# Optimization experiments

Hardware: AMD Instinct MI355X
Metric: run time of the kernel (lower is better)

## Reference

```python
import jax, jax.numpy as jnp
import numpy as np

BAND_WIDTHS = [16]*20 + [32]*12 + [64]*4 + [65]
B, C, F, T, E = 4, 2, 1025, 2048, 128
MAX_BW = 65
D = C * MAX_BW * 2  # padded feature dim (in_channels * max_bandwidth * reim)
EPS = 1e-5


def _band_meta():
    widths = np.asarray(BAND_WIDTHS, np.int32)
    starts = np.concatenate([[0], np.cumsum(widths)[:-1]]).astype(np.int32)
    nb = len(widths)
    bw_mask = (np.arange(MAX_BW)[None, :] < widths[:, None])  # [nb, MAX_BW]
    # feature order per band is (channel, bw, reim), matching torch view_as_real+reshape
    feat_mask = np.broadcast_to(bw_mask[:, None, :, None], (nb, C, MAX_BW, 2)).reshape(nb, D)
    return starts, widths, feat_mask.astype(np.float32)


def setup_inputs() -> dict:
    key = jax.random.key(0)
    ks = jax.random.split(key, 6)
    starts, widths, feat_mask = _band_meta()
    nb = len(widths)
    fm = jnp.asarray(feat_mask)
    x = jax.random.normal(ks[0], (B, C, F, T, 2), jnp.float32)
    ln_gamma = (1.0 + 0.1 * jax.random.normal(ks[1], (nb, D), jnp.float32)) * fm
    ln_beta = 0.1 * jax.random.normal(ks[2], (nb, D), jnp.float32) * fm
    v = 0.05 * jax.random.normal(ks[3], (nb, E, D), jnp.float32) * fm[:, None, :]
    g = 1.0 + 0.1 * jax.random.normal(ks[4], (nb, E), jnp.float32)
    bias = 0.05 * jax.random.normal(ks[5], (nb, E), jnp.float32)
    return {
        "x": x, "ln_gamma": ln_gamma, "ln_beta": ln_beta, "v": v, "g": g,
        "bias": bias, "band_start": jnp.asarray(starts), "band_width": jnp.asarray(widths),
    }


def reference(x, ln_gamma, ln_beta, v, g, bias, band_start, band_width):
    nb = band_start.shape[0]
    # padded gather of each band's frequency slice
    idx = jnp.clip(band_start[:, None] + jnp.arange(MAX_BW)[None, :], 0, F - 1)  # [nb, MAX_BW]
    xb = jnp.take(x, idx, axis=2)               # [B, C, nb, MAX_BW, T, 2]
    xb = jnp.transpose(xb, (0, 2, 4, 1, 3, 5))  # [B, nb, T, C, MAX_BW, 2]
    xb = xb.reshape(B, nb, T, D)
    bw_mask = (jnp.arange(MAX_BW)[None, :] < band_width[:, None])
    fm = jnp.broadcast_to(bw_mask[:, None, :, None], (nb, C, MAX_BW, 2)).reshape(nb, D).astype(x.dtype)
    m = fm[None, :, None, :]                    # [1, nb, 1, D]
    n = (band_width * C * 2).astype(x.dtype)[None, :, None]  # true norm_in per band
    # masked LayerNorm over the valid (ragged) features of each band
    mean = jnp.sum(xb * m, axis=-1) / n         # [B, nb, T]
    diff = (xb - mean[..., None]) * m
    var = jnp.sum(diff * diff, axis=-1) / n
    xhat = diff * jax.lax.rsqrt(var + EPS)[..., None]
    y = (xhat * ln_gamma[None, :, None, :] + ln_beta[None, :, None, :]) * m
    # weight-normalized Linear: W = g * V / ||V||_row (padded cols of V are zero)
    vnorm = jnp.sqrt(jnp.sum(v * v, axis=-1, keepdims=True))  # [nb, E, 1]
    W = g[..., None] * v / vnorm
    z = jnp.einsum("bntd,ned->bnte", y, W) + bias[:, None, :]  # [B, nb, T, E]
    return z
```

## Files before the change

kernel.cpp:

```cpp
#include <hip/hip_runtime.h>
#include <hip/hip_bf16.h>
#include <math.h>

#define NB 37
#define BB 4
#define CC 2
#define FF 1025
#define TT 2048
#define EE 128
#define DD 260
#define EPSF 1e-5f
#define CHS 9

typedef short s16x8 __attribute__((ext_vector_type(8)));
typedef float f32x4 __attribute__((ext_vector_type(4)));
typedef const unsigned int __attribute__((address_space(1))) gu32;
typedef unsigned int __attribute__((address_space(3))) lu32;

__device__ __forceinline__ unsigned short f2bf(float f) {
    unsigned u = __builtin_bit_cast(unsigned, f);
    unsigned r = (u + 0x7FFFu + ((u >> 16) & 1u)) >> 16;
    return (unsigned short)r;
}

__global__ __launch_bounds__(256) void prep_kernel(
    const float* __restrict__ gamma, const float* __restrict__ beta,
    const float* __restrict__ v, const float* __restrict__ g,
    const float* __restrict__ bias, const int* __restrict__ bwidth,
    unsigned short* __restrict__ ATg, float* __restrict__ s1o, float* __restrict__ s2o)
{
    int bid = blockIdx.x;
    int n   = bid >> 4;
    int eg  = bid & 15;
    int tid = threadIdx.x;
    int el  = tid >> 5;
    int kk  = tid & 31;
    int e   = eg * 8 + el;

    int bw    = bwidth[n];
    int Deff  = 4 * bw;
    int twobw = 2 * bw;
    int nCh   = (Deff + 31) >> 5;

    const float* vp = v + (size_t)(n * EE + e) * DD;

    float sq = 0.f;
    for (int d = kk; d < DD; d += 32) { float val = vp[d]; sq = fmaf(val, val, sq); }
    #pragma unroll
    for (int m = 16; m >= 1; m >>= 1) sq += __shfl_xor(sq, m);

    float rv = g[n * EE + e] * rsqrtf(sq);

    float s1 = 0.f, s2 = 0.f;
    unsigned short* Abase = ATg + (size_t)n * CHS * (EE * 32) + e * 32 + kk;
    for (int ch = 0; ch < nCh; ++ch) {
        int k = ch * 32 + kk;
        float a = 0.f;
        if (k < Deff) {
            int d = (k >= twobw) ? (130 + k - twobw) : k;
            float W = rv * vp[d];
            a = gamma[n * DD + d] * W;
            s1 += a;
            s2 = fmaf(beta[n * DD + d], W, s2);
        }
        Abase[(size_t)ch * (EE * 32)] = f2bf(a);
    }
    #pragma unroll
    for (int m = 16; m >= 1; m >>= 1) { s1 += __shfl_xor(s1, m); s2 += __shfl_xor(s2, m); }
    if (kk == 0) {
        s1o[n * EE + e] = s1;
        s2o[n * EE + e] = s2 + bias[n * EE + e];
    }
}

__global__ __launch_bounds__(256) void fused_kernel(
    const float* __restrict__ x, const int* __restrict__ bstart,
    const int* __restrict__ bwidth,
    const unsigned short* __restrict__ ATg, const float* __restrict__ s1a,
    const float* __restrict__ s2a, float* __restrict__ out)
{
    int bid  = blockIdx.x;
    int n    = bid % NB;
    int rest = bid / NB;
    int tt   = rest & 15;
    int b    = rest >> 4;
    int t0   = tt * 128;
    int f0   = bstart[n];
    int bw   = bwidth[n];
    int nPairs = 2 * bw;
    int Deff   = 4 * bw;
    int nChF   = Deff >> 5;
    int remP   = nPairs - nChF * 16;
    int nChT   = nChF + (remP ? 1 : 0);

    int tid   = threadIdx.x;
    int lane  = tid & 63;
    int l15   = lane & 15;
    int ksub  = lane >> 4;
    int wv    = tid >> 6;
    int tband = (wv >> 1) * 64;
    int ewave = (wv & 1) * 64;

    __shared__ __align__(16) float Xs[3 * 4096];

    const char* xbase = (const char*)x;

    auto STAGE = [&](int ch, int bufOff) {
        #pragma unroll
        for (int j = 0; j < 4; ++j) {
            int pl = wv * 4 + j;
            int p  = ch * 16 + pl;
            p = (p < nPairs) ? p : (nPairs - 1);
            int c   = (p >= bw) ? 1 : 0;
            int row = (b * CC + c) * FF + f0 + (p - c * bw);
            const char* gsrc = xbase + (size_t)row * 16384 + (size_t)t0 * 8
                             + (size_t)lane * 16;
            __builtin_amdgcn_global_load_lds(
                (gu32*)gsrc, (lu32*)(Xs + bufOff + pl * 256), 16, 0, 0);
        }
    };

    const s16x8* Ab = reinterpret_cast<const s16x8*>(
        ATg + (size_t)n * CHS * (EE * 32)) + ((ewave + l15) * 4 + ksub);

    f32x4 acc[4][4];
    #pragma unroll
    for (int mi = 0; mi < 4; ++mi)
        #pragma unroll
        for (int ni = 0; ni < 4; ++ni)
            acc[mi][ni] = (f32x4){0.f, 0.f, 0.f, 0.f};
    float sA[4] = {0.f, 0.f, 0.f, 0.f};
    float qA[4] = {0.f, 0.f, 0.f, 0.f};

    STAGE(0, 0);
    STAGE(1, 4096);

    for (int ch = 0; ch < nChT; ++ch) {
        if (ch + 1 < nChT) asm volatile("s_waitcnt vmcnt(4)" ::: "memory");
        else               asm volatile("s_waitcnt vmcnt(0)" ::: "memory");
        __builtin_amdgcn_s_barrier();
        __builtin_amdgcn_sched_barrier(0);

        s16x8 a0 = Ab[ch * 512];
        s16x8 a1 = Ab[ch * 512 + 64];
        s16x8 a2 = Ab[ch * 512 + 128];
        s16x8 a3 = Ab[ch * 512 + 192];

        if (ch + 2 < nChT) STAGE(ch + 2, ((ch + 2) % 3) * 4096);

        const float2* Xp = reinterpret_cast<const float2*>(Xs + (ch % 3) * 4096);
        bool tail = (ch == nChF);

        #pragma unroll
        for (int mi = 0; mi < 4; ++mi) {
            float2 vv[4];
            #pragma unroll
            for (int j = 0; j < 4; ++j)
                vv[j] = Xp[(4 * ksub + j) * 128 + tband + mi * 16 + l15];
            if (tail) {
                #pragma unroll
                for (int j = 0; j < 4; ++j)
                    if (4 * ksub + j >= remP) vv[j] = make_float2(0.f, 0.f);
            }
            float s = 0.f, q = 0.f;
            union { s16x8 v; __hip_bfloat162 h[4]; } afu;
            #pragma unroll
            for (int j = 0; j < 4; ++j) {
                s += vv[j].x + vv[j].y;
                q = fmaf(vv[j].x, vv[j].x, q);
                q = fmaf(vv[j].y, vv[j].y, q);
                afu.h[j] = __float22bfloat162_rn(make_float2(vv[j].x, vv[j].y));
            }
            sA[mi] += s;
            qA[mi] += q;
            s16x8 af = afu.v;
            acc[mi][0] = __builtin_amdgcn_mfma_f32_16x16x32_bf16(af, a0, acc[mi][0], 0, 0, 0);
            acc[mi][1] = __builtin_amdgcn_mfma_f32_16x16x32_bf16(af, a1, acc[mi][1], 0, 0, 0);
            acc[mi][2] = __builtin_amdgcn_mfma_f32_16x16x32_bf16(af, a2, acc[mi][2], 0, 0, 0);
            acc[mi][3] = __builtin_amdgcn_mfma_f32_16x16x32_bf16(af, a3, acc[mi][3], 0, 0, 0);
        }
    }

    float inv = 1.f / (float)Deff;
    float mrow[4][4], rrow[4][4];
    #pragma unroll
    for (int mi = 0; mi < 4; ++mi) {
        float s = sA[mi], q = qA[mi];
        s += __shfl_xor(s, 16); s += __shfl_xor(s, 32);
        q += __shfl_xor(q, 16); q += __shfl_xor(q, 32);
        float mean = s * inv;
        float var  = fmaf(q, inv, -mean * mean);
        float rs   = rsqrtf(var + EPSF);
        #pragma unroll
        for (int j = 0; j < 4; ++j) {
            int src = (ksub << 2) + j;
            mrow[mi][j] = __shfl(mean, src);
            rrow[mi][j] = __shfl(rs, src);
        }
    }

    float s1r[4], s2r[4];
    #pragma unroll
    for (int ni = 0; ni < 4; ++ni) {
        int e = ewave + ni * 16 + l15;
        s1r[ni] = s1a[n * EE + e];
        s2r[ni] = s2a[n * EE + e];
    }
    size_t outRow = ((size_t)(b * NB + n)) * TT;
    #pragma unroll
    for (int mi = 0; mi < 4; ++mi) {
        #pragma unroll
        for (int j = 0; j < 4; ++j) {
            int t = t0 + tband + mi * 16 + (ksub << 2) + j;
            float m = mrow[mi][j], r = rrow[mi][j];
            float* op = out + (outRow + t) * EE + ewave + l15;
            #pragma unroll
            for (int ni = 0; ni < 4; ++ni)
                op[ni * 16] = fmaf(r, acc[mi][ni][j] - m * s1r[ni], s2r[ni]);
        }
    }
}

extern "C" void kernel_launch(void* const* d_in, const int* in_sizes, int n_in,
                              void* d_out, int out_size, void* d_ws, size_t ws_size,
                              hipStream_t stream)
{
    const float* x      = (const float*)d_in[0];
    const float* gamma  = (const float*)d_in[1];
    const float* beta   = (const float*)d_in[2];
    const float* v      = (const float*)d_in[3];
    const float* g      = (const float*)d_in[4];
    const float* bias   = (const float*)d_in[5];
    const int*   bstart = (const int*)d_in[6];
    const int*   bwidth = (const int*)d_in[7];
    float* out = (float*)d_out;

    unsigned short* ATg = (unsigned short*)d_ws;
    float* s1  = (float*)(ATg + (size_t)NB * CHS * EE * 32);
    float* s2p = s1 + NB * EE;

    prep_kernel<<<NB * 16, 256, 0, stream>>>(gamma, beta, v, g, bias, bwidth, ATg, s1, s2p);
    fused_kernel<<<BB * NB * 16, 256, 0, stream>>>(x, bstart, bwidth, ATg, s1, s2p, out);
}
```

Measured before the change: 80.17 us.

## Process two time tiles per block with double-buffered LDS and continuous prefetch

```diff
diff --git a/kernel.cpp b/kernel.cpp
--- a/kernel.cpp
+++ b/kernel.cpp
@@ -73,7 +73,7 @@
     }
 }
 
-__global__ __launch_bounds__(256) void fused_kernel(
+__global__ __launch_bounds__(256, 5) void fused_kernel(
     const float* __restrict__ x, const int* __restrict__ bstart,
     const int* __restrict__ bwidth,
     const unsigned short* __restrict__ ATg, const float* __restrict__ s1a,
@@ -82,9 +82,9 @@
     int bid  = blockIdx.x;
     int n    = bid % NB;
     int rest = bid / NB;
-    int tt   = rest & 15;
-    int b    = rest >> 4;
-    int t0   = tt * 128;
+    int sl   = rest & 7;
+    int b    = rest >> 3;
+    int t0   = sl * 256;
     int f0   = bstart[n];
     int bw   = bwidth[n];
     int nPairs = 2 * bw;
@@ -101,11 +101,11 @@
     int tband = (wv >> 1) * 64;
     int ewave = (wv & 1) * 64;
 
-    __shared__ __align__(16) float Xs[3 * 4096];
+    __shared__ __align__(16) float Xs[2 * 4096];
 
     const char* xbase = (const char*)x;
 
-    auto STAGE = [&](int ch, int bufOff) {
+    auto STAGE = [&](int ts, int ch, int bufOff) {
         #pragma unroll
         for (int j = 0; j < 4; ++j) {
             int pl = wv * 4 + j;
@@ -113,8 +113,8 @@
             p = (p < nPairs) ? p : (nPairs - 1);
             int c   = (p >= bw) ? 1 : 0;
             int row = (b * CC + c) * FF + f0 + (p - c * bw);
-            const char* gsrc = xbase + (size_t)row * 16384 + (size_t)t0 * 8
-                             + (size_t)lane * 16;
+            const char* gsrc = xbase + (size_t)row * 16384
+                             + (size_t)(t0 + ts * 128) * 8 + (size_t)lane * 16;
             __builtin_amdgcn_global_load_lds(
                 (gu32*)gsrc, (lu32*)(Xs + bufOff + pl * 256), 16, 0, 0);
         }
@@ -132,91 +132,99 @@
     float sA[4] = {0.f, 0.f, 0.f, 0.f};
     float qA[4] = {0.f, 0.f, 0.f, 0.f};
 
-    STAGE(0, 0);
-    STAGE(1, 4096);
-
-    for (int ch = 0; ch < nChT; ++ch) {
-        if (ch + 1 < nChT) asm volatile("s_waitcnt vmcnt(4)" ::: "memory");
-        else               asm volatile("s_waitcnt vmcnt(0)" ::: "memory");
-        __builtin_amdgcn_s_barrier();
-        __builtin_amdgcn_sched_barrier(0);
-
-        s16x8 a0 = Ab[ch * 512];
-        s16x8 a1 = Ab[ch * 512 + 64];
-        s16x8 a2 = Ab[ch * 512 + 128];
-        s16x8 a3 = Ab[ch * 512 + 192];
-
-        if (ch + 2 < nChT) STAGE(ch + 2, ((ch + 2) % 3) * 4096);
-
-        const float2* Xp = reinterpret_cast<const float2*>(Xs + (ch % 3) * 4096);
-        bool tail = (ch == nChF);
-
-        #pragma unroll
-        for (int mi = 0; mi < 4; ++mi) {
-            float2 vv[4];
-            #pragma unroll
-            for (int j = 0; j < 4; ++j)
-                vv[j] = Xp[(4 * ksub + j) * 128 + tband + mi * 16 + l15];
-            if (tail) {
+    STAGE(0, 0, 0);
+    int bufOff = 0;
+
+    for (int ts = 0; ts < 2; ++ts) {
+        for (int ch = 0; ch < nChT; ++ch) {
+            asm volatile("s_waitcnt vmcnt(0)" ::: "memory");
+            __builtin_amdgcn_s_barrier();
+            __builtin_amdgcn_sched_barrier(0);
+
+            s16x8 a0 = Ab[ch * 512];
+            s16x8 a1 = Ab[ch * 512 + 64];
+            s16x8 a2 = Ab[ch * 512 + 128];
+            s16x8 a3 = Ab[ch * 512 + 192];
+            __builtin_amdgcn_sched_barrier(0);
+
+            if (ch + 1 < nChT)  STAGE(ts, ch + 1, bufOff ^ 4096);
+            else if (ts == 0)   STAGE(1, 0, bufOff ^ 4096);
+
+            const float2* Xp = reinterpret_cast<const float2*>(Xs + bufOff);
+            bool tail = (ch == nChF);
+
+            #pragma unroll
+            for (int mi = 0; mi < 4; ++mi) {
+                float2 vv[4];
                 #pragma unroll
                 for (int j = 0; j < 4; ++j)
-                    if (4 * ksub + j >= remP) vv[j] = make_float2(0.f, 0.f);
+                    vv[j] = Xp[(4 * ksub + j) * 128 + tband + mi * 16 + l15];
+                if (tail) {
+                    #pragma unroll
+                    for (int j = 0; j < 4; ++j)
+                        if (4 * ksub + j >= remP) vv[j] = make_float2(0.f, 0.f);
+                }
+                float s = 0.f, q = 0.f;
+                union { s16x8 v; __hip_bfloat162 h[4]; } afu;
+                #pragma unroll
+                for (int j = 0; j < 4; ++j) {
+                    s += vv[j].x + vv[j].y;
+                    q = fmaf(vv[j].x, vv[j].x, q);
+                    q = fmaf(vv[j].y, vv[j].y, q);
+                    afu.h[j] = __float22bfloat162_rn(make_float2(vv[j].x, vv[j].y));
+                }
+                sA[mi] += s;
+                qA[mi] += q;
+                s16x8 af = afu.v;
+                acc[mi][0] = __builtin_amdgcn_mfma_f32_16x16x32_bf16(af, a0, acc[mi][0], 0, 0, 0);
+                acc[mi][1] = __builtin_amdgcn_mfma_f32_16x16x32_bf16(af, a1, acc[mi][1], 0, 0, 0);
+                acc[mi][2] = __builtin_amdgcn_mfma_f32_16x16x32_bf16(af, a2, acc[mi][2], 0, 0, 0);
+                acc[mi][3] = __builtin_amdgcn_mfma_f32_16x16x32_bf16(af, a3, acc[mi][3], 0, 0, 0);
             }
-            float s = 0.f, q = 0.f;
-            union { s16x8 v; __hip_bfloat162 h[4]; } afu;
+            bufOff ^= 4096;
+        }
+
+        float inv = 1.f / (float)Deff;
+        float mrow[4][4], rrow[4][4];
+        #pragma unroll
+        for (int mi = 0; mi < 4; ++mi) {
+            float s = sA[mi], q = qA[mi];
+            s += __shfl_xor(s, 16); s += __shfl_xor(s, 32);
+            q += __shfl_xor(q, 16); q += __shfl_xor(q, 32);
+            float mean = s * inv;
+            float var  = fmaf(q, inv, -mean * mean);
+            float rs   = rsqrtf(var + EPSF);
             #pragma unroll
             for (int j = 0; j < 4; ++j) {
-                s += vv[j].x + vv[j].y;
-                q = fmaf(vv[j].x, vv[j].x, q);
-                q = fmaf(vv[j].y, vv[j].y, q);
-                afu.h[j] = __float22bfloat162_rn(make_float2(vv[j].x, vv[j].y));
+                int src = (ksub << 2) + j;
+                mrow[mi][j] = __shfl(mean, src);
+                rrow[mi][j] = __shfl(rs, src);
             }
-            sA[mi] += s;
-            qA[mi] += q;
-            s16x8 af = afu.v;
-            acc[mi][0] = __builtin_amdgcn_mfma_f32_16x16x32_bf16(af, a0, acc[mi][0], 0, 0, 0);
-            acc[mi][1] = __builtin_amdgcn_mfma_f32_16x16x32_bf16(af, a1, acc[mi][1], 0, 0, 0);
-            acc[mi][2] = __builtin_amdgcn_mfma_f32_16x16x32_bf16(af, a2, acc[mi][2], 0, 0, 0);
-            acc[mi][3] = __builtin_amdgcn_mfma_f32_16x16x32_bf16(af, a3, acc[mi][3], 0, 0, 0);
-        }
-    }
-
-    float inv = 1.f / (float)Deff;
-    float mrow[4][4], rrow[4][4];
-    #pragma unroll
-    for (int mi = 0; mi < 4; ++mi) {
-        float s = sA[mi], q = qA[mi];
-        s += __shfl_xor(s, 16); s += __shfl_xor(s, 32);
-        q += __shfl_xor(q, 16); q += __shfl_xor(q, 32);
-        float mean = s * inv;
-        float var  = fmaf(q, inv, -mean * mean);
-        float rs   = rsqrtf(var + EPSF);
-        #pragma unroll
-        for (int j = 0; j < 4; ++j) {
-            int src = (ksub << 2) + j;
-            mrow[mi][j] = __shfl(mean, src);
-            rrow[mi][j] = __shfl(rs, src);
-        }
-    }
-
-    float s1r[4], s2r[4];
-    #pragma unroll
-    for (int ni = 0; ni < 4; ++ni) {
-        int e = ewave + ni * 16 + l15;
-        s1r[ni] = s1a[n * EE + e];
-        s2r[ni] = s2a[n * EE + e];
-    }
-    size_t outRow = ((size_t)(b * NB + n)) * TT;
-    #pragma unroll
-    for (int mi = 0; mi < 4; ++mi) {
-        #pragma unroll
-        for (int j = 0; j < 4; ++j) {
-            int t = t0 + tband + mi * 16 + (ksub << 2) + j;
-            float m = mrow[mi][j], r = rrow[mi][j];
-            float* op = out + (outRow + t) * EE + ewave + l15;
+        }
+
+        float s1r[4], s2r[4];
+        #pragma unroll
+        for (int ni = 0; ni < 4; ++ni) {
+            int e = ewave + ni * 16 + l15;
+            s1r[ni] = s1a[n * EE + e];
+            s2r[ni] = s2a[n * EE + e];
+        }
+        size_t outRow = ((size_t)(b * NB + n)) * TT;
+        #pragma unroll
+        for (int mi = 0; mi < 4; ++mi) {
+            #pragma unroll
+            for (int j = 0; j < 4; ++j) {
+                int t = t0 + ts * 128 + tband + mi * 16 + (ksub << 2) + j;
+                float m = mrow[mi][j], r = rrow[mi][j];
+                float* op = out + (outRow + t) * EE + ewave + l15;
+                #pragma unroll
+                for (int ni = 0; ni < 4; ++ni)
+                    op[ni * 16] = fmaf(r, acc[mi][ni][j] - m * s1r[ni], s2r[ni]);
+            }
             #pragma unroll
             for (int ni = 0; ni < 4; ++ni)
-                op[ni * 16] = fmaf(r, acc[mi][ni][j] - m * s1r[ni], s2r[ni]);
+                acc[mi][ni] = (f32x4){0.f, 0.f, 0.f, 0.f};
+            sA[mi] = 0.f; qA[mi] = 0.f;
         }
     }
 }
@@ -240,5 +248,5 @@
     float* s2p = s1 + NB * EE;
 
     prep_kernel<<<NB * 16, 256, 0, stream>>>(gamma, beta, v, g, bias, bwidth, ATg, s1, s2p);
-    fused_kernel<<<BB * NB * 16, 256, 0, stream>>>(x, bstart, bwidth, ATg, s1, s2p, out);
-}
+    fused_kernel<<<BB * NB * 8, 256, 0, stream>>>(x, bstart, bwidth, ATg, s1, s2p, out);
+}
```

New measurement: 310.7 us. 288% more time.

## Restructure pipeline to double-buffered two-chunk stages with dedicated tail load

Applied to the files above, without the earlier changes.

```diff
diff --git a/kernel.cpp b/kernel.cpp
--- a/kernel.cpp
+++ b/kernel.cpp
@@ -88,10 +88,9 @@
     int f0   = bstart[n];
     int bw   = bwidth[n];
     int nPairs = 2 * bw;
-    int Deff   = 4 * bw;
-    int nChF   = Deff >> 5;
+    int nChF   = (4 * bw) >> 5;
+    int nPairF = nChF >> 1;
     int remP   = nPairs - nChF * 16;
-    int nChT   = nChF + (remP ? 1 : 0);
 
     int tid   = threadIdx.x;
     int lane  = tid & 63;
@@ -101,16 +100,15 @@
     int tband = (wv >> 1) * 64;
     int ewave = (wv & 1) * 64;
 
-    __shared__ __align__(16) float Xs[3 * 4096];
+    __shared__ __align__(16) float Xs[2 * 8192];
 
     const char* xbase = (const char*)x;
 
-    auto STAGE = [&](int ch, int bufOff) {
-        #pragma unroll
-        for (int j = 0; j < 4; ++j) {
-            int pl = wv * 4 + j;
-            int p  = ch * 16 + pl;
-            p = (p < nPairs) ? p : (nPairs - 1);
+    auto STAGE = [&](int cp, int bufOff) {
+        #pragma unroll
+        for (int j = 0; j < 8; ++j) {
+            int pl = wv * 8 + j;
+            int p  = cp * 32 + pl;
             int c   = (p >= bw) ? 1 : 0;
             int row = (b * CC + c) * FF + f0 + (p - c * bw);
             const char* gsrc = xbase + (size_t)row * 16384 + (size_t)t0 * 8
@@ -119,6 +117,20 @@
                 (gu32*)gsrc, (lu32*)(Xs + bufOff + pl * 256), 16, 0, 0);
         }
     };
+    auto STAGE_TAIL = [&](int bufOff) {
+        if (wv == 0) {
+            #pragma unroll
+            for (int j = 0; j < 2; ++j) {
+                int p   = nChF * 16 + j;
+                int c   = (p >= bw) ? 1 : 0;
+                int row = (b * CC + c) * FF + f0 + (p - c * bw);
+                const char* gsrc = xbase + (size_t)row * 16384 + (size_t)t0 * 8
+                                 + (size_t)lane * 16;
+                __builtin_amdgcn_global_load_lds(
+                    (gu32*)gsrc, (lu32*)(Xs + bufOff + j * 256), 16, 0, 0);
+            }
+        }
+    };
 
     const s16x8* Ab = reinterpret_cast<const s16x8*>(
         ATg + (size_t)n * CHS * (EE * 32)) + ((ewave + l15) * 4 + ksub);
@@ -133,34 +145,72 @@
     float qA[4] = {0.f, 0.f, 0.f, 0.f};
 
     STAGE(0, 0);
-    STAGE(1, 4096);
-
-    for (int ch = 0; ch < nChT; ++ch) {
-        if (ch + 1 < nChT) asm volatile("s_waitcnt vmcnt(4)" ::: "memory");
-        else               asm volatile("s_waitcnt vmcnt(0)" ::: "memory");
+    int bufOff = 0;
+
+    for (int cp = 0; cp < nPairF; ++cp) {
+        asm volatile("s_waitcnt vmcnt(0)" ::: "memory");
         __builtin_amdgcn_s_barrier();
         __builtin_amdgcn_sched_barrier(0);
 
-        s16x8 a0 = Ab[ch * 512];
-        s16x8 a1 = Ab[ch * 512 + 64];
-        s16x8 a2 = Ab[ch * 512 + 128];
-        s16x8 a3 = Ab[ch * 512 + 192];
-
-        if (ch + 2 < nChT) STAGE(ch + 2, ((ch + 2) % 3) * 4096);
-
-        const float2* Xp = reinterpret_cast<const float2*>(Xs + (ch % 3) * 4096);
-        bool tail = (ch == nChF);
-
+        int ch0 = 2 * cp;
+        s16x8 a00 = Ab[ch0 * 512];       s16x8 a01 = Ab[ch0 * 512 + 64];
+        s16x8 a02 = Ab[ch0 * 512 + 128]; s16x8 a03 = Ab[ch0 * 512 + 192];
+        s16x8 a10 = Ab[ch0 * 512 + 512]; s16x8 a11 = Ab[ch0 * 512 + 576];
+        s16x8 a12 = Ab[ch0 * 512 + 640]; s16x8 a13 = Ab[ch0 * 512 + 704];
+        __builtin_amdgcn_sched_barrier(0);
+
+        if (cp + 1 < nPairF)       STAGE(cp + 1, bufOff ^ 8192);
+        else if (remP)             STAGE_TAIL(bufOff ^ 8192);
+
+        #pragma unroll
+        for (int cc = 0; cc < 2; ++cc) {
+            const float2* Xp = reinterpret_cast<const float2*>(Xs + bufOff + cc * 4096);
+            s16x8 aw0 = cc ? a10 : a00, aw1 = cc ? a11 : a01;
+            s16x8 aw2 = cc ? a12 : a02, aw3 = cc ? a13 : a03;
+            #pragma unroll
+            for (int mi = 0; mi < 4; ++mi) {
+                float2 vv[4];
+                #pragma unroll
+                for (int j = 0; j < 4; ++j)
+                    vv[j] = Xp[(4 * ksub + j) * 128 + tband + mi * 16 + l15];
+                float s = 0.f, q = 0.f;
+                union { s16x8 v; __hip_bfloat162 h[4]; } afu;
+                #pragma unroll
+                for (int j = 0; j < 4; ++j) {
+                    s += vv[j].x + vv[j].y;
+                    q = fmaf(vv[j].x, vv[j].x, q);
+                    q = fmaf(vv[j].y, vv[j].y, q);
+                    afu.h[j] = __float22bfloat162_rn(make_float2(vv[j].x, vv[j].y));
+                }
+                sA[mi] += s;
+                qA[mi] += q;
+                s16x8 af = afu.v;
+                acc[mi][0] = __builtin_amdgcn_mfma_f32_16x16x32_bf16(af, aw0, acc[mi][0], 0, 0, 0);
+                acc[mi][1] = __builtin_amdgcn_mfma_f32_16x16x32_bf16(af, aw1, acc[mi][1], 0, 0, 0);
+                acc[mi][2] = __builtin_amdgcn_mfma_f32_16x16x32_bf16(af, aw2, acc[mi][2], 0, 0, 0);
+                acc[mi][3] = __builtin_amdgcn_mfma_f32_16x16x32_bf16(af, aw3, acc[mi][3], 0, 0, 0);
+            }
+        }
+        bufOff ^= 8192;
+    }
+
+    if (remP) {
+        asm volatile("s_waitcnt vmcnt(0)" ::: "memory");
+        __builtin_amdgcn_s_barrier();
+        __builtin_amdgcn_sched_barrier(0);
+        int ch = nChF;
+        s16x8 a0 = Ab[ch * 512];       s16x8 a1 = Ab[ch * 512 + 64];
+        s16x8 a2 = Ab[ch * 512 + 128]; s16x8 a3 = Ab[ch * 512 + 192];
+        const float2* Xp = reinterpret_cast<const float2*>(Xs + bufOff);
         #pragma unroll
         for (int mi = 0; mi < 4; ++mi) {
             float2 vv[4];
             #pragma unroll
-            for (int j = 0; j < 4; ++j)
-                vv[j] = Xp[(4 * ksub + j) * 128 + tband + mi * 16 + l15];
-            if (tail) {
-                #pragma unroll
-                for (int j = 0; j < 4; ++j)
-                    if (4 * ksub + j >= remP) vv[j] = make_float2(0.f, 0.f);
+            for (int j = 0; j < 4; ++j) {
+                int pl = 4 * ksub + j;
+                vv[j] = make_float2(0.f, 0.f);
+                if (pl < 2)
+                    vv[j] = Xp[pl * 128 + tband + mi * 16 + l15];
             }
             float s = 0.f, q = 0.f;
             union { s16x8 v; __hip_bfloat162 h[4]; } afu;
@@ -181,7 +231,7 @@
         }
     }
 
-    float inv = 1.f / (float)Deff;
+    float inv = 1.f / (float)(4 * bw);
     float mrow[4][4], rrow[4][4];
     #pragma unroll
     for (int mi = 0; mi < 4; ++mi) {
```

Measured after the change: 78.86 us (median of 2 runs). Within noise of the previous version (-1.6%).
